# Kernel tuning notes

Hardware: AMD Instinct MI355X
Metric: run time of the kernel (lower is better)

## Reference

```python
import jax, jax.numpy as jnp
import numpy as np


def setup_inputs() -> dict:
    key = jax.random.key(0)
    k1, k2, k3, k4, k5 = jax.random.split(key, 5)
    B, TQ, TK, DQ, DV, U = 4, 512, 512, 512, 512, 256
    query = jax.random.normal(k1, (B, TQ, DQ), dtype=jnp.float32)
    value = jax.random.normal(k2, (B, TK, DV), dtype=jnp.float32)
    W1 = jax.random.normal(k3, (DQ, U), dtype=jnp.float32) * (1.0 / np.sqrt(DQ))
    W2 = jax.random.normal(k4, (DV, U), dtype=jnp.float32) * (1.0 / np.sqrt(DV))
    scale = jax.random.normal(k5, (U,), dtype=jnp.float32)
    return {"query": query, "value": value, "W1": W1, "W2": W2, "scale": scale}


def reference(query, value, W1, W2, scale):
    # Dense projections (no bias)
    q = jnp.einsum('bqd,du->bqu', query, W1)   # [B, Tq, U]
    k = jnp.einsum('bkd,du->bku', value, W2)   # [B, Tk, U]
    # Keras AdditiveAttention (use_scale=True):
    # scores[b,q,k] = sum_u scale[u] * tanh(q[b,q,u] + k[b,k,u])
    t = jnp.tanh(q[:, :, None, :] + k[:, None, :, :])  # [B, Tq, Tk, U]
    scores = jnp.einsum('bqku,u->bqk', t, scale)        # [B, Tq, Tk]
    attention_weights = jax.nn.softmax(scores, axis=-1)
    return attention_weights
```

## Files before the change

kernel.cpp:

```cpp
#include <hip/hip_runtime.h>

#define BB 4
#define TQ 512
#define TK 512
#define DQ 512
#define UU 256
#define CSC 2.8853900817779268f
#define L2E 1.4426950408889634f
#define RQ 2

typedef unsigned short u16;
typedef unsigned int u32;
typedef short bf16x8 __attribute__((ext_vector_type(8)));
typedef float f32x4 __attribute__((ext_vector_type(4)));

__device__ __forceinline__ float fexp2(float x) { return __builtin_amdgcn_exp2f(x); }
__device__ __forceinline__ float frcp(float x)  { return __builtin_amdgcn_rcpf(x); }
__device__ __forceinline__ u32 pkhi(u32 a, u32 b) {
    return (b & 0xffff0000u) | (a >> 16);
}

__global__ __launch_bounds__(256) void proj_fused(
    const float* __restrict__ Aq, const float* __restrict__ Av,
    const float* __restrict__ W1, const float* __restrict__ W2,
    float* __restrict__ Eq, float* __restrict__ Ek)
{
    __shared__ __align__(16) char raw[17408];
    u16* As_h = (u16*)raw;
    u16* As_l = (u16*)(raw + 5120);
    float* fin = (float*)raw;

    const int z = blockIdx.z;
    const float* A = z ? Av : Aq;
    const float* W = z ? W2 : W1;

    const int t = threadIdx.x;
    const int m0 = blockIdx.x * 64, n0 = blockIdx.y * 64;
    const int row = t >> 2, kseg = (t & 3) * 8;
    const int wave = t >> 6, ln = t & 15, qd = (t & 63) >> 4;
    const int wm = wave >> 1, wn = wave & 1;

    const size_t abase = (size_t)(m0 + row) * DQ + kseg;
    const int ncol = n0 + wn * 32 + ln;

    f32x4 acc[2][2] = {};

    for (int k0 = 0; k0 < DQ; k0 += 32) {
        const float4 av0 = *(const float4*)&A[abase + k0];
        const float4 av1 = *(const float4*)&A[abase + k0 + 4];
        float wv[2][8];
        #pragma unroll
        for (int j = 0; j < 2; j++) {
            #pragma unroll
            for (int e = 0; e < 8; e++)
                wv[j][e] = W[(size_t)(k0 + qd * 8 + e) * UU + ncol + j * 16];
        }
        __syncthreads();
        {
            const float f[8] = {av0.x, av0.y, av0.z, av0.w, av1.x, av1.y, av1.z, av1.w};
            u32 x[8], lx[8];
            #pragma unroll
            for (int e = 0; e < 8; e++) {
                x[e]  = __float_as_uint(f[e]);
                lx[e] = __float_as_uint(f[e] - __uint_as_float(x[e] & 0xffff0000u));
            }
            uint4 hw, lw;
            hw.x = pkhi(x[0], x[1]);  hw.y = pkhi(x[2], x[3]);
            hw.z = pkhi(x[4], x[5]);  hw.w = pkhi(x[6], x[7]);
            lw.x = pkhi(lx[0], lx[1]); lw.y = pkhi(lx[2], lx[3]);
            lw.z = pkhi(lx[4], lx[5]); lw.w = pkhi(lx[6], lx[7]);
            *(uint4*)&As_h[row * 40 + kseg] = hw;
            *(uint4*)&As_l[row * 40 + kseg] = lw;
        }
        __syncthreads();

        bf16x8 ah[2], al[2], bh[2], bl[2];
        #pragma unroll
        for (int i = 0; i < 2; i++) {
            const int ar = (wm * 32 + i * 16 + ln) * 40 + qd * 8;
            ah[i] = *(const bf16x8*)&As_h[ar];
            al[i] = *(const bf16x8*)&As_l[ar];
        }
        #pragma unroll
        for (int j = 0; j < 2; j++) {
            u32 y[8], ly[8];
            #pragma unroll
            for (int e = 0; e < 8; e++) {
                y[e]  = __float_as_uint(wv[j][e]);
                ly[e] = __float_as_uint(wv[j][e] - __uint_as_float(y[e] & 0xffff0000u));
            }
            union { uint4 u; bf16x8 v; } h, l;
            h.u.x = pkhi(y[0], y[1]);  h.u.y = pkhi(y[2], y[3]);
            h.u.z = pkhi(y[4], y[5]);  h.u.w = pkhi(y[6], y[7]);
            l.u.x = pkhi(ly[0], ly[1]); l.u.y = pkhi(ly[2], ly[3]);
            l.u.z = pkhi(ly[4], ly[5]); l.u.w = pkhi(ly[6], ly[7]);
            bh[j] = h.v; bl[j] = l.v;
        }
        #pragma unroll
        for (int i = 0; i < 2; i++) {
            #pragma unroll
            for (int j = 0; j < 2; j++) {
                acc[i][j] = __builtin_amdgcn_mfma_f32_16x16x32_bf16(ah[i], bh[j], acc[i][j], 0, 0, 0);
                acc[i][j] = __builtin_amdgcn_mfma_f32_16x16x32_bf16(ah[i], bl[j], acc[i][j], 0, 0, 0);
                acc[i][j] = __builtin_amdgcn_mfma_f32_16x16x32_bf16(al[i], bh[j], acc[i][j], 0, 0, 0);
            }
        }
    }

    if (z == 0) {
        #pragma unroll
        for (int i = 0; i < 2; i++) {
            #pragma unroll
            for (int j = 0; j < 2; j++) {
                #pragma unroll
                for (int r = 0; r < 4; r++) {
                    const int m = m0 + wm * 32 + i * 16 + qd * 4 + r;
                    const int n = n0 + wn * 32 + j * 16 + ln;
                    Eq[(size_t)m * UU + n] = fexp2(CSC * acc[i][j][r]);
                }
            }
        }
    } else {
        __syncthreads();
        #pragma unroll
        for (int i = 0; i < 2; i++) {
            #pragma unroll
            for (int j = 0; j < 2; j++) {
                #pragma unroll
                for (int r = 0; r < 4; r++) {
                    const int ml = wm * 32 + i * 16 + qd * 4 + r;
                    const int nl = wn * 32 + j * 16 + ln;
                    fin[ml * 68 + nl] = fexp2(CSC * acc[i][j][r]);
                }
            }
        }
        __syncthreads();
        const int b = m0 >> 9, j0 = m0 & 511;
        #pragma unroll
        for (int i = 0; i < 4; i++) {
            const int idx = i * 256 + t;
            const int jl = idx & 63, u4 = idx >> 6;
            const float4 v = *(const float4*)&fin[jl * 68 + u4 * 4];
            ((float4*)Ek)[(size_t)(b * (UU / 4) + (n0 >> 2) + u4) * TK + j0 + jl] = v;
        }
    }
}

__global__ __launch_bounds__(512) void attn_softmax(
    const float* __restrict__ Eq,
    const float* __restrict__ Ek,
    const float* __restrict__ scale,
    float* __restrict__ out)
{
    __shared__ float redbuf[RQ][8];
    const int t  = threadIdx.x;
    const int b  = blockIdx.x >> 8;
    const int q0 = (blockIdx.x & 255) * RQ;
    const float*  qrow = Eq + (size_t)(b * TQ + q0) * UU;
    const float4* kb4  = (const float4*)Ek + (size_t)b * (UU / 4) * TK + t;

    float acc[RQ] = {};
    float4 kbuf[2];
    kbuf[0] = kb4[0];
    kbuf[1] = kb4[TK];

    #pragma unroll 2
    for (int g = 0; g < UU / 4; g++) {
        const float4 kv = kbuf[g & 1];
        if (g + 2 < UU / 4) kbuf[g & 1] = kb4[(size_t)(g + 2) * TK];
        const float4 sc4 = *(const float4*)&scale[4 * g];
        const float* sf = (const float*)&sc4;
        const float* kf = (const float*)&kv;
        #pragma unroll
        for (int r = 0; r < RQ; r++) {
            const float4 q4 = *(const float4*)&qrow[(size_t)r * UU + 4 * g];
            const float* qf = (const float*)&q4;
            #pragma unroll
            for (int p = 0; p < 4; p++) {
                const float e = qf[p] * kf[p];
                const float d = e + 1.0f;
                acc[r] = fmaf(sf[p], frcp(d), acc[r]);
            }
        }
    }
    #pragma unroll
    for (int r = 0; r < RQ; r++) acc[r] *= -2.0f;

    const int wave = t >> 6, lane = t & 63;
    float m[RQ], p[RQ];

    #pragma unroll
    for (int r = 0; r < RQ; r++) {
        float v = acc[r];
        #pragma unroll
        for (int o = 32; o > 0; o >>= 1) v = fmaxf(v, __shfl_xor(v, o));
        if (lane == 0) redbuf[r][wave] = v;
    }
    __syncthreads();
    #pragma unroll
    for (int r = 0; r < RQ; r++) {
        float v = redbuf[r][0];
        #pragma unroll
        for (int w = 1; w < 8; w++) v = fmaxf(v, redbuf[r][w]);
        m[r] = v;
    }
    __syncthreads();

    #pragma unroll
    for (int r = 0; r < RQ; r++) {
        p[r] = fexp2(L2E * (acc[r] - m[r]));
        float v = p[r];
        #pragma unroll
        for (int o = 32; o > 0; o >>= 1) v += __shfl_xor(v, o);
        if (lane == 0) redbuf[r][wave] = v;
    }
    __syncthreads();
    #pragma unroll
    for (int r = 0; r < RQ; r++) {
        float v = 0.0f;
        #pragma unroll
        for (int w = 0; w < 8; w++) v += redbuf[r][w];
        const float rinv = frcp(v);
        out[(size_t)(b * TQ + q0 + r) * TK + t] = p[r] * rinv;
    }
}

extern "C" void kernel_launch(void* const* d_in, const int* in_sizes, int n_in,
                              void* d_out, int out_size, void* d_ws, size_t ws_size,
                              hipStream_t stream) {
    const float* query = (const float*)d_in[0];
    const float* value = (const float*)d_in[1];
    const float* W1    = (const float*)d_in[2];
    const float* W2    = (const float*)d_in[3];
    const float* scale = (const float*)d_in[4];
    float* out = (float*)d_out;

    float* Eq = (float*)d_ws;
    float* Ek = Eq + (size_t)BB * TQ * UU;
    (void)ws_size;

    proj_fused<<<dim3(32, 4, 2), 256, 0, stream>>>(query, value, W1, W2, Eq, Ek);
    attn_softmax<<<dim3(BB * TQ / RQ), 512, 0, stream>>>(Eq, Ek, scale, out);
}
```

Baseline: 121.3 us.

## Pair reciprocals in attention loop, retile projection GEMM, deepen K prefetch

In the attention kernel, each pair of sigmoid-style terms s0/d0 + s1/d1 is merged into one reciprocal, (s0*d1 + s1*d0)/(d0*d1). This halves the transcendental rcp count on the dominant inner loop. The prefetch ring for Ek grows from two to four float4 slots to hide more load latency. The projection kernel is retiled to 32-row blocks with W staged through shared memory using coalesced float4 loads, doubling the grid. The merged reciprocal risks overflow or precision loss when the product d0*d1 grows large.

Result: slower. 143.1 us (+18.0%).

```diff
diff --git a/kernel.cpp b/kernel.cpp
--- a/kernel.cpp
+++ b/kernel.cpp
@@ -16,108 +16,95 @@
 
 __device__ __forceinline__ float fexp2(float x) { return __builtin_amdgcn_exp2f(x); }
 __device__ __forceinline__ float frcp(float x)  { return __builtin_amdgcn_rcpf(x); }
-__device__ __forceinline__ u32 pkhi(u32 a, u32 b) {
-    return (b & 0xffff0000u) | (a >> 16);
-}
-
-__global__ __launch_bounds__(256) void proj_fused(
+__device__ __forceinline__ u32 pkhi(u32 a, u32 b) { return (b & 0xffff0000u) | (a >> 16); }
+
+__global__ __launch_bounds__(256) void proj2(
     const float* __restrict__ Aq, const float* __restrict__ Av,
     const float* __restrict__ W1, const float* __restrict__ W2,
     float* __restrict__ Eq, float* __restrict__ Ek)
 {
-    __shared__ __align__(16) char raw[17408];
-    u16* As_h = (u16*)raw;
-    u16* As_l = (u16*)(raw + 5120);
-    float* fin = (float*)raw;
+    __shared__ __align__(16) char raw[14336];
+    u16*   As_h = (u16*)raw;
+    u16*   As_l = (u16*)(raw + 2560);
+    float* Ws   = (float*)(raw + 5120);
+    float* fin  = (float*)raw;
 
     const int z = blockIdx.z;
     const float* A = z ? Av : Aq;
     const float* W = z ? W2 : W1;
 
     const int t = threadIdx.x;
-    const int m0 = blockIdx.x * 64, n0 = blockIdx.y * 64;
-    const int row = t >> 2, kseg = (t & 3) * 8;
+    const int m0 = blockIdx.x * 32, n0 = blockIdx.y * 64;
     const int wave = t >> 6, ln = t & 15, qd = (t & 63) >> 4;
-    const int wm = wave >> 1, wn = wave & 1;
-
-    const size_t abase = (size_t)(m0 + row) * DQ + kseg;
-    const int ncol = n0 + wn * 32 + ln;
-
-    f32x4 acc[2][2] = {};
+    const int arow = t >> 3, ak4 = (t & 7) * 4;
+    const int wk = t >> 4, wn4 = (t & 15) * 4;
+
+    f32x4 acc[2] = {};
 
     for (int k0 = 0; k0 < DQ; k0 += 32) {
-        const float4 av0 = *(const float4*)&A[abase + k0];
-        const float4 av1 = *(const float4*)&A[abase + k0 + 4];
-        float wv[2][8];
-        #pragma unroll
-        for (int j = 0; j < 2; j++) {
-            #pragma unroll
-            for (int e = 0; e < 8; e++)
-                wv[j][e] = W[(size_t)(k0 + qd * 8 + e) * UU + ncol + j * 16];
-        }
+        const float4 a4  = *(const float4*)&A[(size_t)(m0 + arow) * DQ + k0 + ak4];
+        const float4 w40 = *(const float4*)&W[(size_t)(k0 + wk) * UU + n0 + wn4];
+        const float4 w41 = *(const float4*)&W[(size_t)(k0 + 16 + wk) * UU + n0 + wn4];
         __syncthreads();
         {
-            const float f[8] = {av0.x, av0.y, av0.z, av0.w, av1.x, av1.y, av1.z, av1.w};
-            u32 x[8], lx[8];
-            #pragma unroll
-            for (int e = 0; e < 8; e++) {
+            const float f[4] = {a4.x, a4.y, a4.z, a4.w};
+            u32 x[4], lx[4];
+            #pragma unroll
+            for (int e = 0; e < 4; e++) {
                 x[e]  = __float_as_uint(f[e]);
                 lx[e] = __float_as_uint(f[e] - __uint_as_float(x[e] & 0xffff0000u));
             }
-            uint4 hw, lw;
+            uint2 hw, lw;
             hw.x = pkhi(x[0], x[1]);  hw.y = pkhi(x[2], x[3]);
-            hw.z = pkhi(x[4], x[5]);  hw.w = pkhi(x[6], x[7]);
             lw.x = pkhi(lx[0], lx[1]); lw.y = pkhi(lx[2], lx[3]);
-            lw.z = pkhi(lx[4], lx[5]); lw.w = pkhi(lx[6], lx[7]);
-            *(uint4*)&As_h[row * 40 + kseg] = hw;
-            *(uint4*)&As_l[row * 40 + kseg] = lw;
-        }
-        __syncthreads();
-
-        bf16x8 ah[2], al[2], bh[2], bl[2];
-        #pragma unroll
-        for (int i = 0; i < 2; i++) {
-            const int ar = (wm * 32 + i * 16 + ln) * 40 + qd * 8;
+            *(uint2*)&As_h[arow * 40 + ak4] = hw;
+            *(uint2*)&As_l[arow * 40 + ak4] = lw;
+        }
+        *(float4*)&Ws[wk * 72 + wn4] = w40;
+        *(float4*)&Ws[(wk + 16) * 72 + wn4] = w41;
+        __syncthreads();
+
+        bf16x8 ah[2], al[2], bh, bl;
+        #pragma unroll
+        for (int i = 0; i < 2; i++) {
+            const int ar = (i * 16 + ln) * 40 + qd * 8;
             ah[i] = *(const bf16x8*)&As_h[ar];
             al[i] = *(const bf16x8*)&As_l[ar];
         }
-        #pragma unroll
-        for (int j = 0; j < 2; j++) {
+        {
+            const int cl = wave * 16 + ln;
+            float wf[8];
+            #pragma unroll
+            for (int e = 0; e < 8; e++) wf[e] = Ws[(qd * 8 + e) * 72 + cl];
             u32 y[8], ly[8];
             #pragma unroll
             for (int e = 0; e < 8; e++) {
-                y[e]  = __float_as_uint(wv[j][e]);
-                ly[e] = __float_as_uint(wv[j][e] - __uint_as_float(y[e] & 0xffff0000u));
+                y[e]  = __float_as_uint(wf[e]);
+                ly[e] = __float_as_uint(wf[e] - __uint_as_float(y[e] & 0xffff0000u));
             }
             union { uint4 u; bf16x8 v; } h, l;
             h.u.x = pkhi(y[0], y[1]);  h.u.y = pkhi(y[2], y[3]);
             h.u.z = pkhi(y[4], y[5]);  h.u.w = pkhi(y[6], y[7]);
             l.u.x = pkhi(ly[0], ly[1]); l.u.y = pkhi(ly[2], ly[3]);
             l.u.z = pkhi(ly[4], ly[5]); l.u.w = pkhi(ly[6], ly[7]);
-            bh[j] = h.v; bl[j] = l.v;
-        }
-        #pragma unroll
-        for (int i = 0; i < 2; i++) {
-            #pragma unroll
-            for (int j = 0; j < 2; j++) {
-                acc[i][j] = __builtin_amdgcn_mfma_f32_16x16x32_bf16(ah[i], bh[j], acc[i][j], 0, 0, 0);
-                acc[i][j] = __builtin_amdgcn_mfma_f32_16x16x32_bf16(ah[i], bl[j], acc[i][j], 0, 0, 0);
-                acc[i][j] = __builtin_amdgcn_mfma_f32_16x16x32_bf16(al[i], bh[j], acc[i][j], 0, 0, 0);
-            }
-        }
-    }
-
+            bh = h.v; bl = l.v;
+        }
+        #pragma unroll
+        for (int i = 0; i < 2; i++) {
+            acc[i] = __builtin_amdgcn_mfma_f32_16x16x32_bf16(ah[i], bh, acc[i], 0, 0, 0);
+            acc[i] = __builtin_amdgcn_mfma_f32_16x16x32_bf16(ah[i], bl, acc[i], 0, 0, 0);
+            acc[i] = __builtin_amdgcn_mfma_f32_16x16x32_bf16(al[i], bh, acc[i], 0, 0, 0);
+        }
+    }
+
+    const int ncol = n0 + wave * 16 + ln;
     if (z == 0) {
         #pragma unroll
         for (int i = 0; i < 2; i++) {
             #pragma unroll
-            for (int j = 0; j < 2; j++) {
-                #pragma unroll
-                for (int r = 0; r < 4; r++) {
-                    const int m = m0 + wm * 32 + i * 16 + qd * 4 + r;
-                    const int n = n0 + wn * 32 + j * 16 + ln;
-                    Eq[(size_t)m * UU + n] = fexp2(CSC * acc[i][j][r]);
-                }
+            for (int r = 0; r < 4; r++) {
+                const int m = m0 + i * 16 + qd * 4 + r;
+                Eq[(size_t)m * UU + ncol] = fexp2(CSC * acc[i][r]);
             }
         }
     } else {
@@ -125,21 +112,18 @@
         #pragma unroll
         for (int i = 0; i < 2; i++) {
             #pragma unroll
-            for (int j = 0; j < 2; j++) {
-                #pragma unroll
-                for (int r = 0; r < 4; r++) {
-                    const int ml = wm * 32 + i * 16 + qd * 4 + r;
-                    const int nl = wn * 32 + j * 16 + ln;
-                    fin[ml * 68 + nl] = fexp2(CSC * acc[i][j][r]);
-                }
+            for (int r = 0; r < 4; r++) {
+                const int ml = i * 16 + qd * 4 + r;
+                const int nl = wave * 16 + ln;
+                fin[ml * 68 + nl] = fexp2(CSC * acc[i][r]);
             }
         }
         __syncthreads();
         const int b = m0 >> 9, j0 = m0 & 511;
         #pragma unroll
-        for (int i = 0; i < 4; i++) {
-            const int idx = i * 256 + t;
-            const int jl = idx & 63, u4 = idx >> 6;
+        for (int p = 0; p < 2; p++) {
+            const int idx = p * 256 + t;
+            const int jl = idx & 31, u4 = idx >> 5;
             const float4 v = *(const float4*)&fin[jl * 68 + u4 * 4];
             ((float4*)Ek)[(size_t)(b * (UU / 4) + (n0 >> 2) + u4) * TK + j0 + jl] = v;
         }
@@ -160,14 +144,14 @@
     const float4* kb4  = (const float4*)Ek + (size_t)b * (UU / 4) * TK + t;
 
     float acc[RQ] = {};
-    float4 kbuf[2];
-    kbuf[0] = kb4[0];
-    kbuf[1] = kb4[TK];
+    float4 kbuf[4];
+    #pragma unroll
+    for (int i = 0; i < 4; i++) kbuf[i] = kb4[(size_t)i * TK];
 
     #pragma unroll 2
     for (int g = 0; g < UU / 4; g++) {
-        const float4 kv = kbuf[g & 1];
-        if (g + 2 < UU / 4) kbuf[g & 1] = kb4[(size_t)(g + 2) * TK];
+        const float4 kv = kbuf[g & 3];
+        if (g + 4 < UU / 4) kbuf[g & 3] = kb4[(size_t)(g + 4) * TK];
         const float4 sc4 = *(const float4*)&scale[4 * g];
         const float* sf = (const float*)&sc4;
         const float* kf = (const float*)&kv;
@@ -176,10 +160,11 @@
             const float4 q4 = *(const float4*)&qrow[(size_t)r * UU + 4 * g];
             const float* qf = (const float*)&q4;
             #pragma unroll
-            for (int p = 0; p < 4; p++) {
-                const float e = qf[p] * kf[p];
-                const float d = e + 1.0f;
-                acc[r] = fmaf(sf[p], frcp(d), acc[r]);
+            for (int p = 0; p < 4; p += 2) {
+                const float d0 = fmaf(qf[p],     kf[p],     1.0f);
+                const float d1 = fmaf(qf[p + 1], kf[p + 1], 1.0f);
+                const float num = fmaf(sf[p], d1, sf[p + 1] * d0);
+                acc[r] = fmaf(num, frcp(d0 * d1), acc[r]);
             }
         }
     }
@@ -239,6 +224,6 @@
     float* Ek = Eq + (size_t)BB * TQ * UU;
     (void)ws_size;
 
-    proj_fused<<<dim3(32, 4, 2), 256, 0, stream>>>(query, value, W1, W2, Eq, Ek);
+    proj2<<<dim3(64, 4, 2), 256, 0, stream>>>(query, value, W1, W2, Eq, Ek);
     attn_softmax<<<dim3(BB * TQ / RQ), 512, 0, stream>>>(Eq, Ek, scale, out);
 }
```
